# Performance work log

Measured on AMD Instinct MI355X. Metric: run time of the kernel, lower is better.

## Reference

```python
import jax, jax.numpy as jnp
import numpy as np

EPS = 1e-5

def _bn(x, g, b, m, v):
    # x: [B, C, S]; per-channel affine batchnorm in eval mode
    scale = (g * jax.lax.rsqrt(v + EPS))[None, :, None]
    return (x - m[None, :, None]) * scale + b[None, :, None]

def setup_inputs() -> dict:
    key = jax.random.key(0)
    ks = jax.random.split(key, 32)
    B, C, H, W = 8, 512, 64, 32
    IC = 64        # inter_channel = 512 // 8
    S = H * W      # in_spatial = 2048
    IS = S // 8    # inter_spatial = 256
    DS = IS // 8   # down = 32
    randn = lambda k, shp: jax.random.normal(k, shp, dtype=jnp.float32)
    rand = lambda k, shp: jax.random.uniform(k, shp, dtype=jnp.float32)
    return {
        'x': randn(ks[0], (B, C, H, W)),
        'Wt': randn(ks[1], (IC, C)) * 0.05,
        'tg': rand(ks[2], (IC,)), 'tb': randn(ks[3], (IC,)) * 0.1,
        'tm': randn(ks[4], (IC,)) * 0.1, 'tv': rand(ks[5], (IC,)),
        'Wp': randn(ks[6], (IC, C)) * 0.05,
        'pg': rand(ks[7], (IC,)), 'pb': randn(ks[8], (IC,)) * 0.1,
        'pm': randn(ks[9], (IC,)) * 0.1, 'pv': rand(ks[10], (IC,)),
        'Wgg': randn(ks[11], (IS, 2 * S)) * 0.02,
        'ggg': rand(ks[12], (IS,)), 'ggb': randn(ks[13], (IS,)) * 0.1,
        'ggm': randn(ks[14], (IS,)) * 0.1, 'ggv': rand(ks[15], (IS,)),
        'W1': randn(ks[16], (DS, IS)) * 0.05,
        'w1g': rand(ks[17], (DS,)), 'w1b': randn(ks[18], (DS,)) * 0.1,
        'w1m': randn(ks[19], (DS,)) * 0.1, 'w1v': rand(ks[20], (DS,)),
        'W2': randn(ks[21], (1, DS)) * 0.1,
        'w2g': rand(ks[22], (1,)), 'w2b': randn(ks[23], (1,)) * 0.1,
        'w2m': randn(ks[24], (1,)) * 0.1, 'w2v': rand(ks[25], (1,)),
    }

def reference(x, Wt, tg, tb, tm, tv, Wp, pg, pb, pm, pv,
              Wgg, ggg, ggb, ggm, ggv, W1, w1g, w1b, w1m, w1v,
              W2, w2g, w2b, w2m, w2v):
    B, C, H, W = x.shape
    S = H * W
    xf = x.reshape(B, C, S)
    # theta / phi: 1x1 conv + BN + ReLU -> [B, IC, S]
    theta = jax.nn.relu(_bn(jnp.einsum('oc,bcs->bos', Wt, xf), tg, tb, tm, tv))
    phi = jax.nn.relu(_bn(jnp.einsum('oc,bcs->bos', Wp, xf), pg, pb, pm, pv))
    # spatial affinity: Gs[b,s,t] = sum_c theta[b,c,s] * phi[b,c,t]
    Gs = jnp.einsum('bcs,bct->bst', theta, phi)          # [B, S, S]
    # Gs_in = Gs^T (channels=phi-spatial), Gs_out = Gs (channels=theta-spatial)
    joint = jnp.concatenate([jnp.swapaxes(Gs, 1, 2), Gs], axis=1)  # [B, 2S, S]
    g = jax.nn.relu(_bn(jnp.einsum('oc,bcs->bos', Wgg, joint), ggg, ggb, ggm, ggv))
    y = jax.nn.relu(_bn(jnp.einsum('oc,bcs->bos', W1, g), w1g, w1b, w1m, w1v))
    ys = _bn(jnp.einsum('oc,bcs->bos', W2, y), w2g, w2b, w2m, w2v)  # [B, 1, S]
    gate = jax.nn.sigmoid(ys).reshape(B, 1, H, W)
    return x * gate
```

## Files before the change

### kernel.cpp

```cpp
#include <hip/hip_runtime.h>
#include <math.h>

#define EPS 1e-5f
#define B_ 8
#define C_ 512
#define S_ 2048
#define IC_ 64
#define IS_ 256
#define DS_ 32

#define SZ_T      (S_*C_/2)
#define OFF_THT_H 1024
#define OFF_THT_L (OFF_THT_H + SZ_T)
#define OFF_PHT_H (OFF_THT_L + SZ_T)
#define OFF_PHT_L (OFF_PHT_H + SZ_T)
#define SZ_A      (2*IS_*C_/2)
#define OFF_A_H   (OFF_PHT_L + SZ_T)
#define OFF_A_L   (OFF_A_H + SZ_A)
#define OFF_G     (OFF_A_L + SZ_A)
#define OFF_AP    OFF_G

using short8 = __attribute__((ext_vector_type(8))) short;
using sh4    = __attribute__((ext_vector_type(4))) short;
using f32x4  = __attribute__((ext_vector_type(4))) float;

__device__ __forceinline__ short f2bf(float f) {
  union { float f; unsigned u; } v; v.f = f;
  unsigned r = v.u + 0x7fffu + ((v.u >> 16) & 1u);
  return (short)(r >> 16);
}
__device__ __forceinline__ float bf2f(short h) {
  union { unsigned u; float f; } v;
  v.u = ((unsigned)(unsigned short)h) << 16;
  return v.f;
}
__device__ __forceinline__ void split8arr(const float* f, short8& hi, short8& lo) {
#pragma unroll
  for (int e = 0; e < 8; ++e) {
    short h = f2bf(f[e]);
    hi[e] = h;
    lo[e] = f2bf(f[e] - bf2f(h));
  }
}
__device__ __forceinline__ void split44(float4 a, float4 b, short8& hi, short8& lo) {
  float f[8] = {a.x, a.y, a.z, a.w, b.x, b.y, b.z, b.w};
  split8arr(f, hi, lo);
}

__global__ __launch_bounds__(512) void k1_mfma(
    const float* __restrict__ x, const float* __restrict__ Wt,
    const float* __restrict__ Wp,
    const float* __restrict__ tg, const float* __restrict__ tb,
    const float* __restrict__ tm, const float* __restrict__ tv,
    const float* __restrict__ pg, const float* __restrict__ pb,
    const float* __restrict__ pm, const float* __restrict__ pv,
    float* __restrict__ ws) {
  __shared__ short xh[64 * 72], xlo[64 * 72];
  __shared__ short wh[2][64 * 72], wlo[2][64 * 72];
  __shared__ float cst_l[256];
  const int tid  = threadIdx.x;
  const int lane = tid & 63;
  const int wv   = tid >> 6;
  const int mat  = wv >> 2, sh = wv & 3;
  const int s0   = blockIdx.x * 64;
  const int b    = blockIdx.y;
  const float* xb = x + (size_t)b * C_ * S_;
  const int xs = tid & 63;
  const int xo = tid >> 6;

  if (tid < 64) {
    float a = tg[tid] * rsqrtf(tv[tid] + EPS);
    cst_l[tid] = a; cst_l[64 + tid] = tb[tid] - tm[tid] * a;
    float ap = pg[tid] * rsqrtf(pv[tid] + EPS);
    cst_l[128 + tid] = ap; cst_l[192 + tid] = pb[tid] - pm[tid] * ap;
  }

  float  xr[8];
  float4 wr[2][2];
  f32x4  acc[4];
#pragma unroll
  for (int i = 0; i < 4; ++i) acc[i] = (f32x4){0.f, 0.f, 0.f, 0.f};

#define K1_PF(KC) do {                                                        \
    _Pragma("unroll")                                                         \
    for (int e = 0; e < 8; ++e)                                               \
      xr[e] = xb[(size_t)((KC) + xo * 8 + e) * S_ + s0 + xs];                 \
    _Pragma("unroll")                                                         \
    for (int p = 0; p < 2; ++p) {                                             \
      int q = tid + p * 512;                                                  \
      int mq = q >> 9, m = (q >> 3) & 63, oct = q & 7;                        \
      const float* Wm = mq ? Wp : Wt;                                         \
      wr[p][0] = *(const float4*)&Wm[(size_t)m * C_ + (KC) + oct * 8];        \
      wr[p][1] = *(const float4*)&Wm[(size_t)m * C_ + (KC) + oct * 8 + 4];    \
    } } while (0)

  K1_PF(0);
  for (int c = 0; c < 8; ++c) {
    if (c) __syncthreads();
    {
      short8 hi, lo; split8arr(xr, hi, lo);
      *(short8*)&xh[xs * 72 + xo * 8]  = hi;
      *(short8*)&xlo[xs * 72 + xo * 8] = lo;
    }
#pragma unroll
    for (int p = 0; p < 2; ++p) {
      int q = tid + p * 512;
      int mq = q >> 9, m = (q >> 3) & 63, oct = q & 7;
      short8 hi, lo; split44(wr[p][0], wr[p][1], hi, lo);
      *(short8*)&wh[mq][m * 72 + oct * 8]  = hi;
      *(short8*)&wlo[mq][m * 72 + oct * 8] = lo;
    }
    __syncthreads();
    if (c < 7) K1_PF((c + 1) * 64);
#pragma unroll
    for (int ks = 0; ks < 2; ++ks) {
      const int ko = ks * 32 + ((lane >> 4) << 3);
      short8 bh, bl, ah[4], al[4];
      {
        int r = (sh * 16 + (lane & 15)) * 72 + ko;
        bh = *(const short8*)&xh[r];
        bl = *(const short8*)&xlo[r];
      }
#pragma unroll
      for (int mi = 0; mi < 4; ++mi) {
        int r = (mi * 16 + (lane & 15)) * 72 + ko;
        ah[mi] = *(const short8*)&wh[mat][r];
        al[mi] = *(const short8*)&wlo[mat][r];
      }
#pragma unroll
      for (int mi = 0; mi < 4; ++mi) {
        acc[mi] = __builtin_amdgcn_mfma_f32_16x16x32_bf16(ah[mi], bh, acc[mi], 0, 0, 0);
        acc[mi] = __builtin_amdgcn_mfma_f32_16x16x32_bf16(ah[mi], bl, acc[mi], 0, 0, 0);
        acc[mi] = __builtin_amdgcn_mfma_f32_16x16x32_bf16(al[mi], bh, acc[mi], 0, 0, 0);
      }
    }
  }
#undef K1_PF
  const float* ac = &cst_l[mat * 128];
  short* outH = (short*)(ws + (mat ? OFF_PHT_H : OFF_THT_H));
  short* outL = (short*)(ws + (mat ? OFF_PHT_L : OFF_THT_L));
  const int s = s0 + sh * 16 + (lane & 15);
#pragma unroll
  for (int mi = 0; mi < 4; ++mi) {
    const int m = mi * 16 + ((lane >> 4) << 2);
    float4 sc4 = *(const float4*)&ac[m];
    float4 bi4 = *(const float4*)&ac[64 + m];
    float vals[4];
    vals[0] = fmaxf(sc4.x * acc[mi][0] + bi4.x, 0.f);
    vals[1] = fmaxf(sc4.y * acc[mi][1] + bi4.y, 0.f);
    vals[2] = fmaxf(sc4.z * acc[mi][2] + bi4.z, 0.f);
    vals[3] = fmaxf(sc4.w * acc[mi][3] + bi4.w, 0.f);
    sh4 qh, ql;
#pragma unroll
    for (int e = 0; e < 4; ++e) {
      short h = f2bf(vals[e]);
      qh[e] = h; ql[e] = f2bf(vals[e] - bf2f(h));
    }
    size_t ix = (size_t)s * C_ + b * IC_ + m;
    *(sh4*)&outH[ix] = qh;
    *(sh4*)&outL[ix] = ql;
  }
}

__global__ __launch_bounds__(256) void k2_mfma(
    const float* __restrict__ Wgg, const float* __restrict__ ws,
    float* __restrict__ Ap) {
  __shared__ short nh[64 * 72], nlo[64 * 72];
  __shared__ short oh[128 * 72], olo[128 * 72];
  const int tid  = threadIdx.x;
  const int lane = tid & 63;
  const int wv   = tid >> 6;
  const int n0    = blockIdx.x * 64;
  const int o_blk = blockIdx.y * 128;
  const int mat   = blockIdx.z >> 3;
  const int part  = blockIdx.z & 7;
  const int t0 = part * 256;
  const short* BmH = (const short*)(ws + (mat ? OFF_THT_H : OFF_PHT_H));
  const short* BmL = (const short*)(ws + (mat ? OFF_THT_L : OFF_PHT_L));
  const int xs = tid & 63;
  const int xo = tid >> 6;

  short8 arh[2], arl[2];
  float4 br[4][2];
  f32x4  acc[4][2];
#pragma unroll
  for (int i = 0; i < 4; ++i)
#pragma unroll
    for (int j = 0; j < 2; ++j) acc[i][j] = (f32x4){0.f, 0.f, 0.f, 0.f};

#define K2_PF(KC) do {                                                        \
    _Pragma("unroll")                                                         \
    for (int h = 0; h < 2; ++h) {                                             \
      int oct = xo + h * 4;                                                   \
      _Pragma("unroll")                                                       \
      for (int e = 0; e < 8; ++e) {                                           \
        size_t ix = (size_t)(t0 + (KC) + oct * 8 + e) * C_ + n0 + xs;         \
        arh[h][e] = BmH[ix];                                                  \
        arl[h][e] = BmL[ix];                                                  \
      }                                                                       \
    }                                                                         \
    _Pragma("unroll")                                                         \
    for (int p = 0; p < 4; ++p) {                                             \
      int q = tid + p * 256;                                                  \
      int o = q >> 3, oct = q & 7;                                            \
      const float* src = &Wgg[(size_t)(o_blk + o) * (2 * S_) + mat * S_ +     \
                              t0 + (KC) + oct * 8];                           \
      br[p][0] = *(const float4*)src;                                         \
      br[p][1] = *(const float4*)(src + 4);                                   \
    } } while (0)

  K2_PF(0);
  for (int c = 0; c < 4; ++c) {
    if (c) __syncthreads();
#pragma unroll
    for (int h = 0; h < 2; ++h) {
      int oct = xo + h * 4;
      *(short8*)&nh[xs * 72 + oct * 8]  = arh[h];
      *(short8*)&nlo[xs * 72 + oct * 8] = arl[h];
    }
#pragma unroll
    for (int p = 0; p < 4; ++p) {
      int q = tid + p * 256;
      int o = q >> 3, oct = q & 7;
      short8 hi, lo; split44(br[p][0], br[p][1], hi, lo);
      *(short8*)&oh[o * 72 + oct * 8]  = hi;
      *(short8*)&olo[o * 72 + oct * 8] = lo;
    }
    __syncthreads();
    if (c < 3) K2_PF((c + 1) * 64);
#pragma unroll
    for (int ks = 0; ks < 2; ++ks) {
      const int ko = ks * 32 + ((lane >> 4) << 3);
      short8 ah[4], al[4], bh[2], bl[2];
#pragma unroll
      for (int ni = 0; ni < 4; ++ni) {
        int r = (ni * 16 + (lane & 15)) * 72 + ko;
        ah[ni] = *(const short8*)&nh[r];
        al[ni] = *(const short8*)&nlo[r];
      }
#pragma unroll
      for (int oj = 0; oj < 2; ++oj) {
        int r = (wv * 32 + oj * 16 + (lane & 15)) * 72 + ko;
        bh[oj] = *(const short8*)&oh[r];
        bl[oj] = *(const short8*)&olo[r];
      }
#pragma unroll
      for (int ni = 0; ni < 4; ++ni)
#pragma unroll
        for (int oj = 0; oj < 2; ++oj) {
          acc[ni][oj] = __builtin_amdgcn_mfma_f32_16x16x32_bf16(
              ah[ni], bh[oj], acc[ni][oj], 0, 0, 0);
          acc[ni][oj] = __builtin_amdgcn_mfma_f32_16x16x32_bf16(
              ah[ni], bl[oj], acc[ni][oj], 0, 0, 0);
          acc[ni][oj] = __builtin_amdgcn_mfma_f32_16x16x32_bf16(
              al[ni], bh[oj], acc[ni][oj], 0, 0, 0);
        }
    }
  }
#undef K2_PF
#pragma unroll
  for (int ni = 0; ni < 4; ++ni) {
    const int nq = n0 + ni * 16 + ((lane >> 4) << 2);
#pragma unroll
    for (int oj = 0; oj < 2; ++oj) {
      int o = o_blk + wv * 32 + oj * 16 + (lane & 15);
      float4 q;
      q.x = acc[ni][oj][0]; q.y = acc[ni][oj][1];
      q.z = acc[ni][oj][2]; q.w = acc[ni][oj][3];
      *(float4*)&Ap[((size_t)(part * 2 + mat) * IS_ + o) * C_ + nq] = q;
    }
  }
}

__global__ __launch_bounds__(256) void k2b_reduce(float* __restrict__ ws) {
  int f = blockIdx.x * 256 + threadIdx.x;
  const float4* ap = (const float4*)(ws + OFF_AP);
  float4 s = ap[f];
#pragma unroll
  for (int p = 1; p < 8; ++p) {
    float4 t = ap[f + p * 65536];
    s.x += t.x; s.y += t.y; s.z += t.z; s.w += t.w;
  }
  float vals[4] = {s.x, s.y, s.z, s.w};
  sh4 h4, l4;
#pragma unroll
  for (int e = 0; e < 4; ++e) {
    short h = f2bf(vals[e]);
    h4[e] = h; l4[e] = f2bf(vals[e] - bf2f(h));
  }
  ((sh4*)(ws + OFF_A_H))[f] = h4;
  ((sh4*)(ws + OFF_A_L))[f] = l4;
}

__global__ __launch_bounds__(256) void k3_mfma(
    float* __restrict__ ws,
    const float* __restrict__ gg, const float* __restrict__ gb,
    const float* __restrict__ gm, const float* __restrict__ gv) {
  __shared__ short th[64 * 72], tlo[64 * 72];
  __shared__ short ohh[128 * 72], olo[128 * 72];
  __shared__ float cstg[512];
  const int tid  = threadIdx.x;
  const int lane = tid & 63;
  const int wv   = tid >> 6;
  const int s0    = blockIdx.x * 64;
  const int o_blk = blockIdx.y * 128;
  const int b     = blockIdx.z;
  const short* AH = (const short*)(ws + OFF_A_H);
  const short* AL = (const short*)(ws + OFF_A_L);

  {
    float a = gg[tid] * rsqrtf(gv[tid] + EPS);
    cstg[tid] = a; cstg[256 + tid] = gb[tid] - gm[tid] * a;
  }

  short8 arh[2], arl[2];
  short8 brh[4], brl[4];
  f32x4  acc[4][2];
#pragma unroll
  for (int i = 0; i < 4; ++i)
#pragma unroll
    for (int j = 0; j < 2; ++j) acc[i][j] = (f32x4){0.f, 0.f, 0.f, 0.f};

#define K3_PF(MAT) do {                                                       \
    const short* TH = (const short*)(ws + ((MAT) ? OFF_PHT_H : OFF_THT_H));   \
    const short* TL = (const short*)(ws + ((MAT) ? OFF_PHT_L : OFF_THT_L));   \
    _Pragma("unroll")                                                         \
    for (int p = 0; p < 2; ++p) {                                             \
      int q = tid + p * 256;                                                  \
      int sl = q >> 3, oct = q & 7;                                           \
      size_t ix = (size_t)(s0 + sl) * C_ + b * IC_ + oct * 8;                 \
      arh[p] = *(const short8*)&TH[ix];                                       \
      arl[p] = *(const short8*)&TL[ix];                                       \
    }                                                                         \
    _Pragma("unroll")                                                         \
    for (int p = 0; p < 4; ++p) {                                             \
      int q = tid + p * 256;                                                  \
      int o = q >> 3, oct = q & 7;                                            \
      size_t ix = ((size_t)(MAT) * IS_ + o_blk + o) * C_ + b * IC_ + oct * 8; \
      brh[p] = *(const short8*)&AH[ix];                                       \
      brl[p] = *(const short8*)&AL[ix];                                       \
    } } while (0)

  K3_PF(0);
  for (int c = 0; c < 2; ++c) {
    if (c) __syncthreads();
#pragma unroll
    for (int p = 0; p < 2; ++p) {
      int q = tid + p * 256;
      int sl = q >> 3, oct = q & 7;
      *(short8*)&th[sl * 72 + oct * 8]  = arh[p];
      *(short8*)&tlo[sl * 72 + oct * 8] = arl[p];
    }
#pragma unroll
    for (int p = 0; p < 4; ++p) {
      int q = tid + p * 256;
      int o = q >> 3, oct = q & 7;
      *(short8*)&ohh[o * 72 + oct * 8] = brh[p];
      *(short8*)&olo[o * 72 + oct * 8] = brl[p];
    }
    __syncthreads();
    if (c < 1) K3_PF(1);
#pragma unroll
    for (int ks = 0; ks < 2; ++ks) {
      const int ko = ks * 32 + ((lane >> 4) << 3);
      short8 ah[4], al[4], bh[2], bl[2];
#pragma unroll
      for (int si = 0; si < 4; ++si) {
        int r = (si * 16 + (lane & 15)) * 72 + ko;
        ah[si] = *(const short8*)&th[r];
        al[si] = *(const short8*)&tlo[r];
      }
#pragma unroll
      for (int oj = 0; oj < 2; ++oj) {
        int r = (wv * 32 + oj * 16 + (lane & 15)) * 72 + ko;
        bh[oj] = *(const short8*)&ohh[r];
        bl[oj] = *(const short8*)&olo[r];
      }
#pragma unroll
      for (int si = 0; si < 4; ++si)
#pragma unroll
        for (int oj = 0; oj < 2; ++oj) {
          acc[si][oj] = __builtin_amdgcn_mfma_f32_16x16x32_bf16(
              ah[si], bh[oj], acc[si][oj], 0, 0, 0);
          acc[si][oj] = __builtin_amdgcn_mfma_f32_16x16x32_bf16(
              ah[si], bl[oj], acc[si][oj], 0, 0, 0);
          acc[si][oj] = __builtin_amdgcn_mfma_f32_16x16x32_bf16(
              al[si], bh[oj], acc[si][oj], 0, 0, 0);
        }
    }
  }
#undef K3_PF
  short* g = (short*)(ws + OFF_G);
#pragma unroll
  for (int oj = 0; oj < 2; ++oj) {
    int o = o_blk + wv * 32 + oj * 16 + (lane & 15);
    float sc = cstg[o], bi = cstg[256 + o];
#pragma unroll
    for (int si = 0; si < 4; ++si) {
      int sq = s0 + si * 16 + ((lane >> 4) << 2);
      sh4 q4;
      q4[0] = f2bf(fmaxf(sc * acc[si][oj][0] + bi, 0.f));
      q4[1] = f2bf(fmaxf(sc * acc[si][oj][1] + bi, 0.f));
      q4[2] = f2bf(fmaxf(sc * acc[si][oj][2] + bi, 0.f));
      q4[3] = f2bf(fmaxf(sc * acc[si][oj][3] + bi, 0.f));
      *(sh4*)&g[((size_t)b * IS_ + o) * S_ + sq] = q4;
    }
  }
}

__global__ __launch_bounds__(512) void k4_fused(
    const float* __restrict__ x, const float* __restrict__ W1,
    const float* __restrict__ W2,
    const float* __restrict__ w1g, const float* __restrict__ w1b,
    const float* __restrict__ w1m, const float* __restrict__ w1v,
    const float* __restrict__ w2g, const float* __restrict__ w2b,
    const float* __restrict__ w2m, const float* __restrict__ w2v,
    const float* __restrict__ ws, float* __restrict__ out) {
  __shared__ float lds_g[128 * 68];
  __shared__ float lds_w[32 * 260];
  __shared__ float lds_y[32 * 65];
  __shared__ float lds_gate[64];
  __shared__ float wc[66];
  const int tid = threadIdx.x;
  const int s0  = blockIdx.x * 64;
  const int b   = blockIdx.y;
  const int s   = tid & 63;
  const int og  = tid >> 6;
  const short* gsrc = (const short*)(ws + OFF_G) + (size_t)b * IS_ * S_;

  if (tid < 32) {
    float a = w1g[tid] * rsqrtf(w1v[tid] + EPS);
    wc[tid] = a; wc[32 + tid] = w1b[tid] - w1m[tid] * a;
  } else if (tid == 32) {
    float a = w2g[0] * rsqrtf(w2v[0] + EPS);
    wc[64] = a; wc[65] = w2b[0] - w2m[0] * a;
  }
#pragma unroll
  for (int j = 0; j < 4; ++j) {
    int f = tid + j * 512;
    int row = f >> 6, c4 = f & 63;
    *(float4*)&lds_w[row * 260 + c4 * 4] =
        *(const float4*)&W1[(size_t)row * IS_ + c4 * 4];
  }
  float acc[4] = {};

  for (int half = 0; half < 2; ++half) {
    __syncthreads();
#pragma unroll
    for (int j = 0; j < 2; ++j) {
      int ridx = tid + j * 512;
      int row = ridx >> 3, oct = ridx & 7;
      short8 v = *(const short8*)&gsrc[(size_t)(half * 128 + row) * S_ +
                                       s0 + oct * 8];
      float4 f0 = make_float4(bf2f(v[0]), bf2f(v[1]), bf2f(v[2]), bf2f(v[3]));
      float4 f1 = make_float4(bf2f(v[4]), bf2f(v[5]), bf2f(v[6]), bf2f(v[7]));
      *(float4*)&lds_g[row * 68 + oct * 8]     = f0;
      *(float4*)&lds_g[row * 68 + oct * 8 + 4] = f1;
    }
    __syncthreads();
#pragma unroll
    for (int c4 = 0; c4 < 32; ++c4) {
      float g0 = lds_g[(c4 * 4 + 0) * 68 + s];
      float g1 = lds_g[(c4 * 4 + 1) * 68 + s];
      float g2 = lds_g[(c4 * 4 + 2) * 68 + s];
      float g3 = lds_g[(c4 * 4 + 3) * 68 + s];
#pragma unroll
      for (int j = 0; j < 4; ++j) {
        const float4 w = *(const float4*)&lds_w[(og * 4 + j) * 260 +
                                                half * 128 + c4 * 4];
        acc[j] += g0 * w.x + g1 * w.y + g2 * w.z + g3 * w.w;
      }
    }
  }
#pragma unroll
  for (int j = 0; j < 4; ++j) {
    int o = og * 4 + j;
    float v = wc[o] * acc[j] + wc[32 + o];
    lds_y[o * 65 + s] = v > 0.f ? v : 0.f;
  }
  __syncthreads();
  if (tid < 64) {
    float sum = 0.f;
#pragma unroll
    for (int c = 0; c < 32; ++c) sum += W2[c] * lds_y[c * 65 + tid];
    float ys = wc[64] * sum + wc[65];
    lds_gate[tid] = 1.f / (1.f + expf(-ys));
  }
  __syncthreads();
  const int l = tid & 63, w = tid >> 6;
  const int q4 = (l & 15) * 4;
  const int cl = w * 4 + (l >> 4);
  const float4 gv = *(const float4*)&lds_gate[q4];
  const float* xb = x + (size_t)b * C_ * S_ + s0;
  float* ob = out + (size_t)b * C_ * S_ + s0;
#pragma unroll
  for (int it = 0; it < 16; ++it) {
    int ch = it * 32 + cl;
    const float4 xv = *(const float4*)&xb[(size_t)ch * S_ + q4];
    float4 ov;
    ov.x = xv.x * gv.x; ov.y = xv.y * gv.y;
    ov.z = xv.z * gv.z; ov.w = xv.w * gv.w;
    *(float4*)&ob[(size_t)ch * S_ + q4] = ov;
  }
}

extern "C" void kernel_launch(void* const* d_in, const int* in_sizes, int n_in,
                              void* d_out, int out_size, void* d_ws, size_t ws_size,
                              hipStream_t stream) {
  const float* x   = (const float*)d_in[0];
  const float* Wt  = (const float*)d_in[1];
  const float* tg  = (const float*)d_in[2];
  const float* tb  = (const float*)d_in[3];
  const float* tm  = (const float*)d_in[4];
  const float* tv  = (const float*)d_in[5];
  const float* Wp  = (const float*)d_in[6];
  const float* pg  = (const float*)d_in[7];
  const float* pb  = (const float*)d_in[8];
  const float* pm  = (const float*)d_in[9];
  const float* pv  = (const float*)d_in[10];
  const float* Wgg = (const float*)d_in[11];
  const float* ggg = (const float*)d_in[12];
  const float* ggb = (const float*)d_in[13];
  const float* ggm = (const float*)d_in[14];
  const float* ggv = (const float*)d_in[15];
  const float* W1  = (const float*)d_in[16];
  const float* w1g = (const float*)d_in[17];
  const float* w1b = (const float*)d_in[18];
  const float* w1m = (const float*)d_in[19];
  const float* w1v = (const float*)d_in[20];
  const float* W2  = (const float*)d_in[21];
  const float* w2g = (const float*)d_in[22];
  const float* w2b = (const float*)d_in[23];
  const float* w2m = (const float*)d_in[24];
  const float* w2v = (const float*)d_in[25];
  float* ws  = (float*)d_ws;
  float* out = (float*)d_out;

  k1_mfma<<<dim3(32, 8), 512, 0, stream>>>(
      x, Wt, Wp, tg, tb, tm, tv, pg, pb, pm, pv, ws);
  k2_mfma<<<dim3(8, 2, 16), 256, 0, stream>>>(Wgg, ws, ws + OFF_AP);
  k2b_reduce<<<256, 256, 0, stream>>>(ws);
  k3_mfma<<<dim3(32, 2, 8), 256, 0, stream>>>(ws, ggg, ggb, ggm, ggv);
  k4_fused<<<dim3(32, 8), 512, 0, stream>>>(
      x, W1, W2, w1g, w1b, w1m, w1v, w2g, w2b, w2m, w2v, ws, out);
}
```

Before: 69.73 us.

## Fuse split-K reduction into k2 via last-block atomic counter; halve k4 tile

Removes the separate k2b_reduce launch. Each group of eight partial-sum blocks in k2 now bumps an atomic counter, which k1 zeroes, and the last block to arrive sums the partials and writes the hi/lo bf16 split. Separately, k4 now uses 32-column spatial tiles and twice as many blocks, for more parallelism in the gate and apply stage. The fused reduction does its loads and stores with scalar, less coalesced accesses and needs threadfences, and only the last block per group does that extra work.

New measurement: 101.6 us. +45.6%, slower.

```diff
diff --git a/kernel.cpp b/kernel.cpp
--- a/kernel.cpp
+++ b/kernel.cpp
@@ -68,6 +68,9 @@
   const int xs = tid & 63;
   const int xo = tid >> 6;
 
+  if (blockIdx.x == 0 && blockIdx.y == 0 && tid < 32)
+    ((int*)ws)[tid] = 0;
+
   if (tid < 64) {
     float a = tg[tid] * rsqrtf(tv[tid] + EPS);
     cst_l[tid] = a; cst_l[64 + tid] = tb[tid] - tm[tid] * a;
@@ -163,10 +166,11 @@
 }
 
 __global__ __launch_bounds__(256) void k2_mfma(
-    const float* __restrict__ Wgg, const float* __restrict__ ws,
+    const float* __restrict__ Wgg, float* __restrict__ ws,
     float* __restrict__ Ap) {
   __shared__ short nh[64 * 72], nlo[64 * 72];
   __shared__ short oh[128 * 72], olo[128 * 72];
+  __shared__ int lastFlag;
   const int tid  = threadIdx.x;
   const int lane = tid & 63;
   const int wv   = tid >> 6;
@@ -270,26 +274,29 @@
       *(float4*)&Ap[((size_t)(part * 2 + mat) * IS_ + o) * C_ + nq] = q;
     }
   }
-}
-
-__global__ __launch_bounds__(256) void k2b_reduce(float* __restrict__ ws) {
-  int f = blockIdx.x * 256 + threadIdx.x;
-  const float4* ap = (const float4*)(ws + OFF_AP);
-  float4 s = ap[f];
-#pragma unroll
-  for (int p = 1; p < 8; ++p) {
-    float4 t = ap[f + p * 65536];
-    s.x += t.x; s.y += t.y; s.z += t.z; s.w += t.w;
-  }
-  float vals[4] = {s.x, s.y, s.z, s.w};
-  sh4 h4, l4;
-#pragma unroll
-  for (int e = 0; e < 4; ++e) {
-    short h = f2bf(vals[e]);
-    h4[e] = h; l4[e] = f2bf(vals[e] - bf2f(h));
-  }
-  ((sh4*)(ws + OFF_A_H))[f] = h4;
-  ((sh4*)(ws + OFF_A_L))[f] = l4;
+  __threadfence();
+  if (tid == 0) {
+    int grp = mat * 16 + blockIdx.y * 8 + blockIdx.x;
+    int old = atomicAdd((int*)ws + grp, 1);
+    lastFlag = (old == 7);
+  }
+  __syncthreads();
+  if (lastFlag) {
+    __threadfence();
+    short* AH = (short*)(ws + OFF_A_H);
+    short* AL = (short*)(ws + OFF_A_L);
+    for (int e = tid; e < 128 * 64; e += 256) {
+      int o = o_blk + (e >> 6), n = n0 + (e & 63);
+      float s = 0.f;
+#pragma unroll
+      for (int p = 0; p < 8; ++p)
+        s += Ap[((size_t)(p * 2 + mat) * IS_ + o) * C_ + n];
+      short h = f2bf(s);
+      size_t ix = ((size_t)mat * IS_ + o) * C_ + n;
+      AH[ix] = h;
+      AL[ix] = f2bf(s - bf2f(h));
+    }
+  }
 }
 
 __global__ __launch_bounds__(256) void k3_mfma(
@@ -416,16 +423,16 @@
     const float* __restrict__ w2g, const float* __restrict__ w2b,
     const float* __restrict__ w2m, const float* __restrict__ w2v,
     const float* __restrict__ ws, float* __restrict__ out) {
-  __shared__ float lds_g[128 * 68];
+  __shared__ float lds_g[128 * 36];
   __shared__ float lds_w[32 * 260];
-  __shared__ float lds_y[32 * 65];
-  __shared__ float lds_gate[64];
+  __shared__ float lds_y[32 * 33];
+  __shared__ float lds_gate[32];
   __shared__ float wc[66];
   const int tid = threadIdx.x;
-  const int s0  = blockIdx.x * 64;
+  const int s0  = blockIdx.x * 32;
   const int b   = blockIdx.y;
-  const int s   = tid & 63;
-  const int og  = tid >> 6;
+  const int s   = tid & 31;
+  const int og  = tid >> 5;
   const short* gsrc = (const short*)(ws + OFF_G) + (size_t)b * IS_ * S_;
 
   if (tid < 32) {
@@ -442,60 +449,58 @@
     *(float4*)&lds_w[row * 260 + c4 * 4] =
         *(const float4*)&W1[(size_t)row * IS_ + c4 * 4];
   }
-  float acc[4] = {};
+  float acc[2] = {};
 
   for (int half = 0; half < 2; ++half) {
     __syncthreads();
-#pragma unroll
-    for (int j = 0; j < 2; ++j) {
-      int ridx = tid + j * 512;
-      int row = ridx >> 3, oct = ridx & 7;
+    {
+      int row = tid >> 2, oct = tid & 3;
       short8 v = *(const short8*)&gsrc[(size_t)(half * 128 + row) * S_ +
                                        s0 + oct * 8];
       float4 f0 = make_float4(bf2f(v[0]), bf2f(v[1]), bf2f(v[2]), bf2f(v[3]));
       float4 f1 = make_float4(bf2f(v[4]), bf2f(v[5]), bf2f(v[6]), bf2f(v[7]));
-      *(float4*)&lds_g[row * 68 + oct * 8]     = f0;
-      *(float4*)&lds_g[row * 68 + oct * 8 + 4] = f1;
+      *(float4*)&lds_g[row * 36 + oct * 8]     = f0;
+      *(float4*)&lds_g[row * 36 + oct * 8 + 4] = f1;
     }
     __syncthreads();
 #pragma unroll
     for (int c4 = 0; c4 < 32; ++c4) {
-      float g0 = lds_g[(c4 * 4 + 0) * 68 + s];
-      float g1 = lds_g[(c4 * 4 + 1) * 68 + s];
-      float g2 = lds_g[(c4 * 4 + 2) * 68 + s];
-      float g3 = lds_g[(c4 * 4 + 3) * 68 + s];
-#pragma unroll
-      for (int j = 0; j < 4; ++j) {
-        const float4 w = *(const float4*)&lds_w[(og * 4 + j) * 260 +
+      float g0 = lds_g[(c4 * 4 + 0) * 36 + s];
+      float g1 = lds_g[(c4 * 4 + 1) * 36 + s];
+      float g2 = lds_g[(c4 * 4 + 2) * 36 + s];
+      float g3 = lds_g[(c4 * 4 + 3) * 36 + s];
+#pragma unroll
+      for (int j = 0; j < 2; ++j) {
+        const float4 w = *(const float4*)&lds_w[(og * 2 + j) * 260 +
                                                 half * 128 + c4 * 4];
         acc[j] += g0 * w.x + g1 * w.y + g2 * w.z + g3 * w.w;
       }
     }
   }
 #pragma unroll
-  for (int j = 0; j < 4; ++j) {
-    int o = og * 4 + j;
+  for (int j = 0; j < 2; ++j) {
+    int o = og * 2 + j;
     float v = wc[o] * acc[j] + wc[32 + o];
-    lds_y[o * 65 + s] = v > 0.f ? v : 0.f;
+    lds_y[o * 33 + s] = v > 0.f ? v : 0.f;
   }
   __syncthreads();
-  if (tid < 64) {
+  if (tid < 32) {
     float sum = 0.f;
 #pragma unroll
-    for (int c = 0; c < 32; ++c) sum += W2[c] * lds_y[c * 65 + tid];
+    for (int c = 0; c < 32; ++c) sum += W2[c] * lds_y[c * 33 + tid];
     float ys = wc[64] * sum + wc[65];
     lds_gate[tid] = 1.f / (1.f + expf(-ys));
   }
   __syncthreads();
   const int l = tid & 63, w = tid >> 6;
-  const int q4 = (l & 15) * 4;
-  const int cl = w * 4 + (l >> 4);
+  const int q4 = (l & 7) * 4;
+  const int cl = w * 8 + (l >> 3);
   const float4 gv = *(const float4*)&lds_gate[q4];
   const float* xb = x + (size_t)b * C_ * S_ + s0;
   float* ob = out + (size_t)b * C_ * S_ + s0;
 #pragma unroll
-  for (int it = 0; it < 16; ++it) {
-    int ch = it * 32 + cl;
+  for (int it = 0; it < 8; ++it) {
+    int ch = it * 64 + cl;
     const float4 xv = *(const float4*)&xb[(size_t)ch * S_ + q4];
     float4 ov;
     ov.x = xv.x * gv.x; ov.y = xv.y * gv.y;
@@ -539,8 +544,7 @@
   k1_mfma<<<dim3(32, 8), 512, 0, stream>>>(
       x, Wt, Wp, tg, tb, tm, tv, pg, pb, pm, pv, ws);
   k2_mfma<<<dim3(8, 2, 16), 256, 0, stream>>>(Wgg, ws, ws + OFF_AP);
-  k2b_reduce<<<256, 256, 0, stream>>>(ws);
   k3_mfma<<<dim3(32, 2, 8), 256, 0, stream>>>(ws, ggg, ggb, ggm, ggv);
-  k4_fused<<<dim3(32, 8), 512, 0, stream>>>(
+  k4_fused<<<dim3(64, 8), 512, 0, stream>>>(
       x, W1, W2, w1g, w1b, w1m, w1v, w2g, w2b, w2m, w2v, ws, out);
 }
```
